# Performance work log

Hardware: AMD Instinct MI355X
Metric: run time of the kernel (lower is better)

Reference implementation:

```python
import jax, jax.numpy as jnp
import numpy as np
import math

B, S, HID = 1, 2048, 2048
H, KVH, HD = 16, 4, 128
LEVEL = 256


def _rope_tables(seq_len, dim, dtype=jnp.float32):
    inv_freq = 1.0 / (10000.0 ** (np.arange(0, dim, 2, dtype=np.float32) / dim))
    ang = np.arange(seq_len, dtype=np.float32)[:, None] * inv_freq[None, :]  # [S, HD/2]
    emb = np.concatenate([ang, ang], axis=-1)  # [S, HD]
    return jnp.asarray(np.cos(emb), dtype)[None], jnp.asarray(np.sin(emb), dtype)[None]


def setup_inputs() -> dict:
    key = jax.random.key(0)
    ks = jax.random.split(key, 6)
    hidden_states = jax.random.normal(ks[0], (B, S, HID), jnp.float32)
    w_std = 1.0 / math.sqrt(HID)
    Wq = jax.random.normal(ks[1], (H * HD, HID), jnp.float32) * w_std
    Wk = jax.random.normal(ks[2], (KVH * HD, HID), jnp.float32) * w_std
    Wv = jax.random.normal(ks[3], (KVH * HD, HID), jnp.float32) * w_std
    Wo = jax.random.normal(ks[4], (HID, H * HD), jnp.float32) * w_std
    cos, sin = _rope_tables(S, HD)
    # additive causal mask [1,1,S,S]
    tri = jnp.tril(jnp.ones((S, S), jnp.bool_))
    attention_mask = jnp.where(tri, 0.0, -1e9).astype(jnp.float32)[None, None]
    return {
        "hidden_states": hidden_states,
        "Wq": Wq, "Wk": Wk, "Wv": Wv, "Wo": Wo,
        "s_q": jnp.full((1,), 0.05, jnp.float32),
        "s_k": jnp.full((1,), 0.05, jnp.float32),
        "s_v": jnp.full((1,), 0.05, jnp.float32),
        "s_attn": jnp.full((1,), 0.004, jnp.float32),
        "s_out": jnp.full((1,), 0.02, jnp.float32),
        "cos": cos, "sin": sin,
        "attention_mask": attention_mask,
    }


def _lsq(x, s, level, sym):
    # LSQ fake-quant: learned per-tensor step s, STE round, LSQ grad-scale on s.
    if sym:
        qn, qp = -level // 2, level // 2 - 1
    else:
        qn, qp = 0, level - 1
    g = 1.0 / math.sqrt(x.size * qp)          # LSQ gradient scale (static)
    s = jnp.abs(s)
    s_eff = s * g + jax.lax.stop_gradient(s - s * g)  # fwd = s, bwd grad *= g
    v = jnp.clip(x / s_eff, qn, qp)
    q = v + jax.lax.stop_gradient(jnp.round(v) - v)   # STE round
    return q * s_eff


def _rotate_half(x):
    x1, x2 = jnp.split(x, 2, axis=-1)
    return jnp.concatenate([-x2, x1], axis=-1)


def _attn_fwd(hidden_states, Wq, Wk, Wv, Wo, s_q, s_k, s_v, s_attn, s_out,
              cos, sin, attention_mask):
    b, s_len, _ = hidden_states.shape
    # projections -> [B, heads, S, HD]
    q = (hidden_states @ Wq.T).reshape(b, s_len, H, HD).transpose(0, 2, 1, 3)
    q = _lsq(q, s_q, LEVEL, sym=True)
    k = (hidden_states @ Wk.T).reshape(b, s_len, KVH, HD).transpose(0, 2, 1, 3)
    k = _lsq(k, s_k, LEVEL, sym=True)
    v = (hidden_states @ Wv.T).reshape(b, s_len, KVH, HD).transpose(0, 2, 1, 3)
    v = _lsq(v, s_v, LEVEL, sym=True)
    # RoPE (after quant, matching source order)
    c, si = cos[:, None], sin[:, None]  # [B,1,S,HD]
    q = q * c + _rotate_half(q) * si
    k = k * c + _rotate_half(k) * si
    # GQA repeat
    groups = H // KVH
    k = jnp.repeat(k, groups, axis=1)
    v = jnp.repeat(v, groups, axis=1)
    scores = jnp.einsum("bhqd,bhkd->bhqk", q, k) / math.sqrt(HD)
    scores = scores + attention_mask[:, :, :, :s_len]
    attn = jax.nn.softmax(scores.astype(jnp.float32), axis=-1).astype(q.dtype)
    attn = _lsq(attn, s_attn, LEVEL, sym=False)
    out = jnp.einsum("bhqk,bhkd->bhqd", attn, v)
    out = _lsq(out, s_out, LEVEL, sym=False)
    out = out.transpose(0, 2, 1, 3).reshape(b, s_len, H * HD)
    out = out @ Wo.T
    return out, attn


def reference(hidden_states, Wq, Wk, Wv, Wo, s_q, s_k, s_v, s_attn, s_out,
              cos, sin, attention_mask):
    return _attn_fwd(hidden_states, Wq, Wk, Wv, Wo, s_q, s_k, s_v, s_attn,
                     s_out, cos, sin, attention_mask)
```

## Files before the change

kernel.cpp:

```cpp
#include <hip/hip_runtime.h>
#include <math.h>

#define S_LEN 2048
#define HID_DIM 2048
#define NH 16
#define NKVH 4
#define HD 128
#define QD (NH*HD)
#define KD (NKVH*HD)
#define NQKV 3072

typedef _Float16 half8_t __attribute__((ext_vector_type(8)));
typedef _Float16 half4_t __attribute__((ext_vector_type(4)));
typedef float f32x4 __attribute__((ext_vector_type(4)));

#define BM 128
#define BN 128
#define BK 32

typedef const __attribute__((address_space(1))) char gas_char;
typedef __attribute__((address_space(3))) char las_char;
#define GL16(gp, lp) __builtin_amdgcn_global_load_lds((gas_char*)(gp), (las_char*)(lp), 16, 0, 0)

template<int LA, int LB, bool AF32>
__global__ __launch_bounds__(256)
void gemm_f16(const void* __restrict__ Ap, const _Float16* __restrict__ Alo,
              int lda, long long strA,
              const _Float16* __restrict__ Bhi, const _Float16* __restrict__ Blo,
              int ldb, long long strB, int divB,
              void* __restrict__ Cp, int ldc, long long strC,
              int K, float scale_c, const float* sc1, const float* sc2,
              const float* preAp,
              int qmode, const float* q1, const float* q2, const float* q3,
              int causal, int triK)
{
    int bz = blockIdx.z;
    int m0 = blockIdx.y * BM, n0 = blockIdx.x * BN;
    if (causal && n0 > m0 + (BM - 1)) return;
    int Keff = K;
    if (triK && (m0 + BM) < Keff) Keff = m0 + BM;

    const _Float16* Ahi = AF32 ? nullptr : (const _Float16*)Ap + bz * strA;
    const _Float16* AloP = (LA == 2) ? Alo + bz * strA : nullptr;
    const float* Af = AF32 ? (const float*)Ap + bz * strA : nullptr;
    const _Float16* BhiP = Bhi + (long long)(bz / divB) * strB;
    const _Float16* BloP = (LB == 2) ? Blo + (long long)(bz / divB) * strB : nullptr;
    float* Cf = (float*)Cp + bz * strC;
    _Float16* Ch = (_Float16*)Cp + bz * strC;

    float preA = 1.f;
    if (AF32) preA = 1.f / fabsf(preAp[0]);

    __shared__ _Float16 lds[(LA + LB) * 4096];
    _Float16* As0 = lds;
    _Float16* As1 = lds + 4096;
    _Float16* Bs0 = lds + LA * 4096;
    _Float16* Bs1 = lds + (LA + 1) * 4096;

    int t = threadIdx.x;
    int srow = t >> 2;
    int gsw = (srow >> 1) & 3;
    int gc = ((t & 3) ^ gsw) * 8;
    int w = t >> 6, lane = t & 63;
    int wm = (w >> 1) * 64, wn = (w & 1) * 64;
    int lr = lane & 15, lg = lane >> 4;
    int fco = ((lg ^ ((lr >> 1) & 3))) * 8;

    f32x4 acc[4][4];
    #pragma unroll
    for (int i = 0; i < 4; ++i)
        #pragma unroll
        for (int j = 0; j < 4; ++j)
            acc[i][j] = (f32x4){0.f, 0.f, 0.f, 0.f};

    for (int k0 = 0; k0 < Keff; k0 += BK) {
        f32x4 aF[2][2];
        if constexpr (AF32) {
            #pragma unroll
            for (int rep = 0; rep < 2; ++rep) {
                long long ai = (long long)(m0 + rep * 64 + srow) * lda + k0 + gc;
                aF[rep][0] = *(const f32x4*)&Af[ai];
                aF[rep][1] = *(const f32x4*)&Af[ai + 4];
            }
        }
        __syncthreads();
        #pragma unroll
        for (int rep = 0; rep < 2; ++rep) {
            int row = rep * 64 + srow;
            int lo = rep * 2048 + t * 8;
            if constexpr (!AF32) {
                long long ai = (long long)(m0 + row) * lda + k0 + gc;
                GL16(Ahi + ai, As0 + lo);
                if constexpr (LA == 2) GL16(AloP + ai, As1 + lo);
            }
            long long bi = (long long)(n0 + row) * ldb + k0 + gc;
            GL16(BhiP + bi, Bs0 + lo);
            if constexpr (LB == 2) GL16(BloP + bi, Bs1 + lo);
        }
        if constexpr (AF32) {
            #pragma unroll
            for (int rep = 0; rep < 2; ++rep) {
                half8_t h;
                #pragma unroll
                for (int e = 0; e < 4; ++e) {
                    h[e]     = (_Float16)(aF[rep][0][e] * preA);
                    h[e + 4] = (_Float16)(aF[rep][1][e] * preA);
                }
                *(half8_t*)&As0[rep * 2048 + t * 8] = h;
            }
        }
        __syncthreads();

        half8_t a0[4], b0[4];
        #pragma unroll
        for (int i = 0; i < 4; ++i) a0[i] = *(const half8_t*)&As0[(wm + i*16 + lr) * 32 + fco];
        #pragma unroll
        for (int j = 0; j < 4; ++j) b0[j] = *(const half8_t*)&Bs0[(wn + j*16 + lr) * 32 + fco];
        #pragma unroll
        for (int i = 0; i < 4; ++i)
            #pragma unroll
            for (int j = 0; j < 4; ++j)
                acc[i][j] = __builtin_amdgcn_mfma_f32_16x16x32_f16(a0[i], b0[j], acc[i][j], 0, 0, 0);
        if constexpr (LB == 2) {
            half8_t b1[4];
            #pragma unroll
            for (int j = 0; j < 4; ++j) b1[j] = *(const half8_t*)&Bs1[(wn + j*16 + lr) * 32 + fco];
            #pragma unroll
            for (int i = 0; i < 4; ++i)
                #pragma unroll
                for (int j = 0; j < 4; ++j)
                    acc[i][j] = __builtin_amdgcn_mfma_f32_16x16x32_f16(a0[i], b1[j], acc[i][j], 0, 0, 0);
        }
        if constexpr (LA == 2) {
            half8_t a1[4];
            #pragma unroll
            for (int i = 0; i < 4; ++i) a1[i] = *(const half8_t*)&As1[(wm + i*16 + lr) * 32 + fco];
            #pragma unroll
            for (int i = 0; i < 4; ++i)
                #pragma unroll
                for (int j = 0; j < 4; ++j)
                    acc[i][j] = __builtin_amdgcn_mfma_f32_16x16x32_f16(a1[i], b0[j], acc[i][j], 0, 0, 0);
        }
    }

    float se = scale_c;
    if (sc1) se *= fabsf(sc1[0]);
    if (sc2) se *= fabsf(sc2[0]);
    float sv = 1.f;
    if (qmode == 3) {
        const float* sp = (n0 < 2048) ? q1 : ((n0 < 2560) ? q2 : q3);
        sv = fabsf(sp[0]);
        qmode = 1;
    } else if (qmode) {
        sv = fabsf(q1[0]);
    }

    #pragma unroll
    for (int i = 0; i < 4; ++i)
        #pragma unroll
        for (int j = 0; j < 4; ++j)
            #pragma unroll
            for (int r = 0; r < 4; ++r) {
                long long row = m0 + wm + i * 16 + lg * 4 + r;
                long long col = n0 + wn + j * 16 + lr;
                float v = acc[i][j][r] * se;
                if (qmode == 0) {
                    Cf[row * (long long)ldc + col] = v;
                } else if (qmode == 1) {
                    float u = rintf(fminf(fmaxf(v / sv, -128.f), 127.f));
                    Ch[row * (long long)ldc + col] = (_Float16)u;
                } else {
                    float u = rintf(fminf(fmaxf(v / sv, 0.f), 255.f));
                    Ch[row * (long long)ldc + col] = (_Float16)u;
                }
            }
}

__global__ __launch_bounds__(256)
void scores_direct(const _Float16* __restrict__ qhi, const _Float16* __restrict__ qlo,
                   const _Float16* __restrict__ khi, const _Float16* __restrict__ klo,
                   float* __restrict__ attn, float* __restrict__ pml,
                   const float* sq_p, const float* sk_p)
{
    int m0 = blockIdx.y * BM, n0 = blockIdx.x * BN;
    if (n0 > m0 + (BM - 1)) return;
    int h = blockIdx.z;

    const _Float16* Qh = qhi + (long long)h * S_LEN * HD;
    const _Float16* Ql = qlo + (long long)h * S_LEN * HD;
    const _Float16* Kh = khi + (long long)(h >> 2) * S_LEN * HD;
    const _Float16* Kl = klo + (long long)(h >> 2) * S_LEN * HD;
    float* S = attn + (long long)h * S_LEN * S_LEN;

    float se = fabsf(sq_p[0]) * fabsf(sk_p[0]) * 0.08838834764831845f;

    int t = threadIdx.x;
    int w = t >> 6, lane = t & 63;
    int wm = (w >> 1) * 64, wn = (w & 1) * 64;
    int lr = lane & 15, lg = lane >> 4;

    f32x4 acc[4][4];
    #pragma unroll
    for (int i = 0; i < 4; ++i)
        #pragma unroll
        for (int j = 0; j < 4; ++j)
            acc[i][j] = (f32x4){0.f, 0.f, 0.f, 0.f};

    #pragma unroll 1
    for (int ks = 0; ks < 4; ++ks) {
        int kc = ks * 32 + lg * 8;
        half8_t a0[4], a1[4], b0[4], b1[4];
        #pragma unroll
        for (int i = 0; i < 4; ++i) {
            long long ai = (long long)(m0 + wm + i * 16 + lr) * HD + kc;
            a0[i] = *(const half8_t*)&Qh[ai];
            a1[i] = *(const half8_t*)&Ql[ai];
        }
        #pragma unroll
        for (int j = 0; j < 4; ++j) {
            long long bi = (long long)(n0 + wn + j * 16 + lr) * HD + kc;
            b0[j] = *(const half8_t*)&Kh[bi];
            b1[j] = *(const half8_t*)&Kl[bi];
        }
        #pragma unroll
        for (int i = 0; i < 4; ++i)
            #pragma unroll
            for (int j = 0; j < 4; ++j)
                acc[i][j] = __builtin_amdgcn_mfma_f32_16x16x32_f16(a0[i], b0[j], acc[i][j], 0, 0, 0);
        #pragma unroll
        for (int i = 0; i < 4; ++i)
            #pragma unroll
            for (int j = 0; j < 4; ++j)
                acc[i][j] = __builtin_amdgcn_mfma_f32_16x16x32_f16(a0[i], b1[j], acc[i][j], 0, 0, 0);
        #pragma unroll
        for (int i = 0; i < 4; ++i)
            #pragma unroll
            for (int j = 0; j < 4; ++j)
                acc[i][j] = __builtin_amdgcn_mfma_f32_16x16x32_f16(a1[i], b0[j], acc[i][j], 0, 0, 0);
    }

    int cb64 = (n0 + wn) >> 6;
    #pragma unroll
    for (int i = 0; i < 4; ++i)
        #pragma unroll
        for (int r = 0; r < 4; ++r) {
            int row = m0 + wm + i * 16 + lg * 4 + r;
            float vv[4];
            float mloc = -INFINITY;
            #pragma unroll
            for (int j = 0; j < 4; ++j) {
                int col = n0 + wn + j * 16 + lr;
                float v = acc[i][j][r] * se;
                S[(long long)row * S_LEN + col] = v;
                vv[j] = (col <= row) ? v : -INFINITY;
                mloc = fmaxf(mloc, vv[j]);
            }
            #pragma unroll
            for (int o = 1; o < 16; o <<= 1) mloc = fmaxf(mloc, __shfl_xor(mloc, o));
            float sloc = 0.f;
            #pragma unroll
            for (int j = 0; j < 4; ++j) sloc += expf(vv[j] - mloc);
            #pragma unroll
            for (int o = 1; o < 16; o <<= 1) sloc += __shfl_xor(sloc, o);
            if (lr == 0) {
                long long idx = (((long long)h * S_LEN + row) * 32 + cb64) * 2;
                pml[idx] = mloc;
                pml[idx + 1] = sloc;
            }
        }
}

__global__ __launch_bounds__(256)
void reduce_ml(const float* __restrict__ pml, float* __restrict__ fml)
{
    int id = blockIdx.x * 256 + threadIdx.x;
    int r = id & (S_LEN - 1);
    int nb = (r >> 6) + 1;
    float m = -INFINITY, l = 0.f;
    const float* p = pml + (long long)id * 64;
    for (int cb = 0; cb < nb; ++cb) {
        float mp = p[cb * 2], lp = p[cb * 2 + 1];
        float mn = fmaxf(m, mp);
        l = l * expf(m - mn) + lp * expf(mp - mn);
        m = mn;
    }
    fml[id * 2] = m;
    fml[id * 2 + 1] = l;
}

__global__ __launch_bounds__(256)
void finalize_quant(float* __restrict__ attn, const float* __restrict__ fml,
                    const float* __restrict__ s_at_p)
{
    int row = blockIdx.x;
    int q = row & (S_LEN - 1);
    float* p = attn + (long long)row * S_LEN;
    float m = fml[row * 2];
    float l = fml[row * 2 + 1];
    float sa = fabsf(s_at_p[0]);
    int t = threadIdx.x;
    int n4 = (q + 4) & ~3;
    for (int c = t * 4; c < n4; c += 1024) {
        f32x4 v = *(const f32x4*)&p[c];
        f32x4 o;
        #pragma unroll
        for (int e = 0; e < 4; ++e) {
            float u = 0.f;
            if (c + e <= q) {
                float pr = expf(v[e] - m) / l;
                u = rintf(fminf(fmaxf(pr / sa, 0.f), 255.f));
            }
            o[e] = u * sa;
        }
        *(f32x4*)&p[c] = o;
    }
    f32x4 z = (f32x4){0.f, 0.f, 0.f, 0.f};
    for (int c = n4 + t * 4; c < S_LEN; c += 1024)
        *(f32x4*)&p[c] = z;
}

__global__ void split_f16(const float* __restrict__ in, _Float16* __restrict__ hi,
                          _Float16* __restrict__ lo, int n4)
{
    int i = blockIdx.x * 256 + threadIdx.x;
    if (i >= n4) return;
    f32x4 v = ((const f32x4*)in)[i];
    half4_t h, l;
    #pragma unroll
    for (int e = 0; e < 4; ++e) {
        h[e] = (_Float16)v[e];
        l[e] = (_Float16)(v[e] - (float)h[e]);
    }
    ((half4_t*)hi)[i] = h;
    ((half4_t*)lo)[i] = l;
}

__global__ void rope_f16(const _Float16* __restrict__ codes, int ldc_, int colOff,
                         const float* __restrict__ cosT,
                         const float* __restrict__ sinT,
                         _Float16* __restrict__ ohi, _Float16* __restrict__ olo, int nh)
{
    long long idx = (long long)blockIdx.x * 256 + threadIdx.x;
    int d = idx & (HD - 1);
    long long tt = idx >> 7;
    int h = (int)(tt % nh);
    int s = (int)(tt / nh);
    long long base = (long long)s * ldc_ + colOff + h * HD;
    float x = (float)codes[base + d];
    float other = (d < 64) ? -(float)codes[base + d + 64] : (float)codes[base + d - 64];
    float o = x * cosT[s * HD + d] + other * sinT[s * HD + d];
    _Float16 hf = (_Float16)o;
    long long oi = ((long long)h * S_LEN + s) * HD + d;
    ohi[oi] = hf;
    olo[oi] = (_Float16)(o - (float)hf);
}

__global__ __launch_bounds__(256)
void transpose_vf16(const _Float16* __restrict__ in, _Float16* __restrict__ outp)
{
    __shared__ _Float16 tile[64][72];
    int s0 = blockIdx.x * 64, d0 = blockIdx.y * 64, h = blockIdx.z;
    int t = threadIdx.x;
    int rr = t >> 4, cc = (t & 15) * 4;
    #pragma unroll
    for (int r = 0; r < 4; ++r) {
        half4_t v = *(const half4_t*)&in[(long long)(s0 + rr + 16*r) * NQKV + 2560 + h * HD + d0 + cc];
        *(half4_t*)&tile[rr + 16*r][cc] = v;
    }
    __syncthreads();
    #pragma unroll
    for (int r = 0; r < 4; ++r) {
        int dr = rr + 16 * r;
        half4_t o = { tile[cc+0][dr], tile[cc+1][dr], tile[cc+2][dr], tile[cc+3][dr] };
        *(half4_t*)&outp[((long long)h * HD + d0 + dr) * S_LEN + s0 + cc] = o;
    }
}

extern "C" void kernel_launch(void* const* d_in, const int* in_sizes, int n_in,
                              void* d_out, int out_size, void* d_ws, size_t ws_size,
                              hipStream_t stream)
{
    const float* hs    = (const float*)d_in[0];
    const float* Wq    = (const float*)d_in[1];
    const float* Wk    = (const float*)d_in[2];
    const float* Wv    = (const float*)d_in[3];
    const float* Wo    = (const float*)d_in[4];
    const float* s_q   = (const float*)d_in[5];
    const float* s_k   = (const float*)d_in[6];
    const float* s_v   = (const float*)d_in[7];
    const float* s_at  = (const float*)d_in[8];
    const float* s_out = (const float*)d_in[9];
    const float* cosT  = (const float*)d_in[10];
    const float* sinT  = (const float*)d_in[11];

    float* out  = (float*)d_out;
    float* attn = out + (long long)S_LEN * HID_DIM;

    const long long M1 = 1LL * 1024 * 1024;
    const long long M4 = 4LL * M1;
    const long long M6 = 6LL * M1;

    _Float16* wsh   = (_Float16*)d_ws;
    _Float16* qr_hi = wsh;
    _Float16* qr_lo = qr_hi + M4;
    _Float16* kr_hi = qr_lo + M4;
    _Float16* kr_lo = kr_hi + M1;
    _Float16* vT    = kr_lo + M1;
    _Float16* ao    = vT + M1;
    _Float16* Wo_hi = ao + M4;
    _Float16* Wo_lo = Wo_hi + M4;

    _Float16* sc      = (_Float16*)attn;
    _Float16* hs_hi   = sc;
    _Float16* hs_lo   = hs_hi + M4;
    _Float16* Whi     = hs_lo + M4;
    _Float16* Wlo     = Whi + M6;
    _Float16* qkvcode = Wlo + M6;

    float* pml = out;
    float* fml = out + 2LL * 1024 * 1024;

    dim3 blk(256);

    split_f16<<<4096, blk, 0, stream>>>(hs, hs_hi, hs_lo, 1024*1024);
    split_f16<<<4096, blk, 0, stream>>>(Wq, Whi, Wlo, 1024*1024);
    split_f16<<<1024, blk, 0, stream>>>(Wk, Whi + 2048LL*2048, Wlo + 2048LL*2048, 256*1024);
    split_f16<<<1024, blk, 0, stream>>>(Wv, Whi + 2560LL*2048, Wlo + 2560LL*2048, 256*1024);
    split_f16<<<4096, blk, 0, stream>>>(Wo, Wo_hi, Wo_lo, 1024*1024);

    gemm_f16<2,2,false><<<dim3(NQKV/BN, S_LEN/BM, 1), blk, 0, stream>>>(
        hs_hi, hs_lo, HID_DIM, 0, Whi, Wlo, HID_DIM, 0, 1,
        qkvcode, NQKV, 0, HID_DIM, 1.f, nullptr, nullptr, nullptr,
        3, s_q, s_k, s_v, 0, 0);

    rope_f16<<<(NH*S_LEN*HD)/256, blk, 0, stream>>>(qkvcode, NQKV, 0, cosT, sinT, qr_hi, qr_lo, NH);
    rope_f16<<<(NKVH*S_LEN*HD)/256, blk, 0, stream>>>(qkvcode, NQKV, 2048, cosT, sinT, kr_hi, kr_lo, NKVH);
    transpose_vf16<<<dim3(S_LEN/64, HD/64, NKVH), blk, 0, stream>>>(qkvcode, vT);

    scores_direct<<<dim3(S_LEN/BN, S_LEN/BM, NH), blk, 0, stream>>>(
        qr_hi, qr_lo, kr_hi, kr_lo, attn, pml, s_q, s_k);

    reduce_ml<<<(NH*S_LEN)/256, blk, 0, stream>>>(pml, fml);

    finalize_quant<<<NH*S_LEN, blk, 0, stream>>>(attn, fml, s_at);

    gemm_f16<1,1,true><<<dim3(1, S_LEN/BM, NH), blk, 0, stream>>>(
        attn, nullptr, S_LEN, (long long)S_LEN*S_LEN,
        vT, nullptr, S_LEN, (long long)HD*S_LEN, NH/NKVH,
        ao, QD, HD,
        S_LEN, 1.f, s_at, s_v, s_at, 2, s_out, nullptr, nullptr, 0, 1);

    gemm_f16<1,2,false><<<dim3(HID_DIM/BN, S_LEN/BM, 1), blk, 0, stream>>>(
        ao, nullptr, QD, 0, Wo_hi, Wo_lo, QD, 0, 1,
        out, HID_DIM, 0, QD, 1.f, s_out, nullptr, nullptr,
        0, nullptr, nullptr, nullptr, 0, 0);
}
```

Measured before the change: 577.0 us.

## Stage scores tiles through swizzled LDS and coalesce score stores

The scores kernel now loads Q/K hi/lo tiles into swizzled shared memory with direct global-to-LDS loads instead of each wave reading global memory directly. The fp32 score tile is written back through an LDS staging buffer in two halves so that global stores become row-contiguous float4 writes. It also swaps expf for the faster __expf in the scores, reduce and finalize kernels. This adds extra barriers and LDS traffic, and the fast exp carries slight accuracy risk near quantization rounding boundaries.

After: 504.1 us. 1.14x faster.

```diff
diff --git a/kernel.cpp b/kernel.cpp
--- a/kernel.cpp
+++ b/kernel.cpp
@@ -177,27 +177,37 @@
 }
 
 __global__ __launch_bounds__(256)
-void scores_direct(const _Float16* __restrict__ qhi, const _Float16* __restrict__ qlo,
-                   const _Float16* __restrict__ khi, const _Float16* __restrict__ klo,
-                   float* __restrict__ attn, float* __restrict__ pml,
-                   const float* sq_p, const float* sk_p)
+void scores_gemm(const _Float16* __restrict__ qhi, const _Float16* __restrict__ qlo,
+                 const _Float16* __restrict__ khi, const _Float16* __restrict__ klo,
+                 float* __restrict__ attn, float* __restrict__ pml,
+                 const float* sq_p, const float* sk_p)
 {
     int m0 = blockIdx.y * BM, n0 = blockIdx.x * BN;
     if (n0 > m0 + (BM - 1)) return;
     int h = blockIdx.z;
 
-    const _Float16* Qh = qhi + (long long)h * S_LEN * HD;
-    const _Float16* Ql = qlo + (long long)h * S_LEN * HD;
-    const _Float16* Kh = khi + (long long)(h >> 2) * S_LEN * HD;
-    const _Float16* Kl = klo + (long long)(h >> 2) * S_LEN * HD;
+    const _Float16* Ahi = qhi + (long long)h * S_LEN * HD;
+    const _Float16* Alo = qlo + (long long)h * S_LEN * HD;
+    const _Float16* Bhi = khi + (long long)(h >> 2) * S_LEN * HD;
+    const _Float16* Blo = klo + (long long)(h >> 2) * S_LEN * HD;
     float* S = attn + (long long)h * S_LEN * S_LEN;
 
     float se = fabsf(sq_p[0]) * fabsf(sk_p[0]) * 0.08838834764831845f;
 
+    __shared__ float lds_f[8448];
+    _Float16* As0 = (_Float16*)lds_f;
+    _Float16* As1 = As0 + 4096;
+    _Float16* Bs0 = As0 + 8192;
+    _Float16* Bs1 = As0 + 12288;
+
     int t = threadIdx.x;
+    int srow = t >> 2;
+    int gsw = (srow >> 1) & 3;
+    int gc = ((t & 3) ^ gsw) * 8;
     int w = t >> 6, lane = t & 63;
     int wm = (w >> 1) * 64, wn = (w & 1) * 64;
     int lr = lane & 15, lg = lane >> 4;
+    int fco = ((lg ^ ((lr >> 1) & 3))) * 8;
 
     f32x4 acc[4][4];
     #pragma unroll
@@ -206,21 +216,31 @@
         for (int j = 0; j < 4; ++j)
             acc[i][j] = (f32x4){0.f, 0.f, 0.f, 0.f};
 
-    #pragma unroll 1
-    for (int ks = 0; ks < 4; ++ks) {
-        int kc = ks * 32 + lg * 8;
-        half8_t a0[4], a1[4], b0[4], b1[4];
+    for (int k0 = 0; k0 < HD; k0 += BK) {
+        __syncthreads();
+        #pragma unroll
+        for (int rep = 0; rep < 2; ++rep) {
+            int row = rep * 64 + srow;
+            int lo = rep * 2048 + t * 8;
+            long long ai = (long long)(m0 + row) * HD + k0 + gc;
+            long long bi = (long long)(n0 + row) * HD + k0 + gc;
+            GL16(Ahi + ai, As0 + lo);
+            GL16(Alo + ai, As1 + lo);
+            GL16(Bhi + bi, Bs0 + lo);
+            GL16(Blo + bi, Bs1 + lo);
+        }
+        __syncthreads();
+
+        half8_t a0[4], b0[4], a1[4], b1[4];
         #pragma unroll
         for (int i = 0; i < 4; ++i) {
-            long long ai = (long long)(m0 + wm + i * 16 + lr) * HD + kc;
-            a0[i] = *(const half8_t*)&Qh[ai];
-            a1[i] = *(const half8_t*)&Ql[ai];
+            a0[i] = *(const half8_t*)&As0[(wm + i*16 + lr) * 32 + fco];
+            a1[i] = *(const half8_t*)&As1[(wm + i*16 + lr) * 32 + fco];
         }
         #pragma unroll
         for (int j = 0; j < 4; ++j) {
-            long long bi = (long long)(n0 + wn + j * 16 + lr) * HD + kc;
-            b0[j] = *(const half8_t*)&Kh[bi];
-            b1[j] = *(const half8_t*)&Kl[bi];
+            b0[j] = *(const half8_t*)&Bs0[(wn + j*16 + lr) * 32 + fco];
+            b1[j] = *(const half8_t*)&Bs1[(wn + j*16 + lr) * 32 + fco];
         }
         #pragma unroll
         for (int i = 0; i < 4; ++i)
@@ -251,7 +271,6 @@
             for (int j = 0; j < 4; ++j) {
                 int col = n0 + wn + j * 16 + lr;
                 float v = acc[i][j][r] * se;
-                S[(long long)row * S_LEN + col] = v;
                 vv[j] = (col <= row) ? v : -INFINITY;
                 mloc = fmaxf(mloc, vv[j]);
             }
@@ -259,7 +278,7 @@
             for (int o = 1; o < 16; o <<= 1) mloc = fmaxf(mloc, __shfl_xor(mloc, o));
             float sloc = 0.f;
             #pragma unroll
-            for (int j = 0; j < 4; ++j) sloc += expf(vv[j] - mloc);
+            for (int j = 0; j < 4; ++j) sloc += __expf(vv[j] - mloc);
             #pragma unroll
             for (int o = 1; o < 16; o <<= 1) sloc += __shfl_xor(sloc, o);
             if (lr == 0) {
@@ -268,6 +287,30 @@
                 pml[idx + 1] = sloc;
             }
         }
+
+    int r_own = wm >> 6;
+    int lrow = t >> 5;
+    int lcol = (t & 31) * 4;
+    #pragma unroll
+    for (int half = 0; half < 2; ++half) {
+        __syncthreads();
+        if (r_own == half) {
+            #pragma unroll
+            for (int i = 0; i < 4; ++i)
+                #pragma unroll
+                for (int j = 0; j < 4; ++j)
+                    #pragma unroll
+                    for (int r = 0; r < 4; ++r)
+                        lds_f[(i * 16 + lg * 4 + r) * 132 + wn + j * 16 + lr] = acc[i][j][r] * se;
+        }
+        __syncthreads();
+        #pragma unroll
+        for (int it = 0; it < 8; ++it) {
+            int row = it * 8 + lrow;
+            f32x4 v = *(const f32x4*)&lds_f[row * 132 + lcol];
+            *(f32x4*)&S[(long long)(m0 + half * 64 + row) * S_LEN + n0 + lcol] = v;
+        }
+    }
 }
 
 __global__ __launch_bounds__(256)
@@ -281,7 +324,7 @@
     for (int cb = 0; cb < nb; ++cb) {
         float mp = p[cb * 2], lp = p[cb * 2 + 1];
         float mn = fmaxf(m, mp);
-        l = l * expf(m - mn) + lp * expf(mp - mn);
+        l = l * __expf(m - mn) + lp * __expf(mp - mn);
         m = mn;
     }
     fml[id * 2] = m;
@@ -307,7 +350,7 @@
         for (int e = 0; e < 4; ++e) {
             float u = 0.f;
             if (c + e <= q) {
-                float pr = expf(v[e] - m) / l;
+                float pr = __expf(v[e] - m) / l;
                 u = rintf(fminf(fmaxf(pr / sa, 0.f), 255.f));
             }
             o[e] = u * sa;
@@ -437,7 +480,7 @@
     rope_f16<<<(NKVH*S_LEN*HD)/256, blk, 0, stream>>>(qkvcode, NQKV, 2048, cosT, sinT, kr_hi, kr_lo, NKVH);
     transpose_vf16<<<dim3(S_LEN/64, HD/64, NKVH), blk, 0, stream>>>(qkvcode, vT);
 
-    scores_direct<<<dim3(S_LEN/BN, S_LEN/BM, NH), blk, 0, stream>>>(
+    scores_gemm<<<dim3(S_LEN/BN, S_LEN/BM, NH), blk, 0, stream>>>(
         qr_hi, qr_lo, kr_hi, kr_lo, attn, pml, s_q, s_k);
 
     reduce_ml<<<(NH*S_LEN)/256, blk, 0, stream>>>(pml, fml);
```
